# Kernel optimization log

Hardware: AMD Instinct MI355X
Metric: run time of the kernel (lower is better)

The kernel has to match this reference:

```python
import jax, jax.numpy as jnp
import numpy as np

N_S = 4096      # number of sentences
N_K = 8192      # number of knowledge entries
HID = 1024      # settings.hidden_dim
SENT = 1024     # settings.sent_dim


def setup_inputs() -> dict:
    key = jax.random.key(0)
    ks = jax.random.split(key, 6)
    sentences = jax.random.normal(ks[0], (N_S, SENT), dtype=jnp.float32)
    knowledge = jax.random.normal(ks[1], (N_K, 3 * HID), dtype=jnp.float32)
    # Linear params stored as [in, out] for x @ W + b
    Ws = jax.random.normal(ks[2], (SENT, HID), dtype=jnp.float32) * 0.02
    bs = jnp.zeros((HID,), dtype=jnp.float32)
    Wk = jax.random.normal(ks[3], (3 * HID, HID), dtype=jnp.float32) * 0.02
    bk = jnp.zeros((HID,), dtype=jnp.float32)
    return {"sentences": sentences, "knowledge": knowledge,
            "Ws": Ws, "bs": bs, "Wk": Wk, "bk": bk}


def reference(sentences, knowledge, Ws, bs, Wk, bk):
    S = sentences @ Ws + bs                  # [N_s, h]
    K = knowledge @ Wk + bk                  # [N_k, h]
    align_scores = S @ K.T                   # [N_s, N_k]
    # NOTE: softmax over dim=0 (sentence axis), exactly as the torch module
    attentions = jax.nn.softmax(align_scores, axis=0)
    fused = attentions @ knowledge           # [N_s, 3h]
    return (fused, attentions)
```

## Files before the change

kernel.cpp:

```cpp
#include <hip/hip_runtime.h>
#include <hip/hip_bf16.h>
#include <cstdint>
#include <cstddef>

#define N_S 4096
#define N_Kn 8192
#define HID 1024
#define SENT 1024
#define K3 3072

typedef __attribute__((ext_vector_type(4))) float f4;
typedef __attribute__((ext_vector_type(8))) short bf8;
typedef __attribute__((ext_vector_type(4))) short bf4;
typedef unsigned short u16;

__device__ __forceinline__ u16 f2bf(float x) {
    __hip_bfloat16 h = __float2bfloat16(x);
    return __builtin_bit_cast(u16, h);
}
__device__ __forceinline__ float bf2f(u16 u) {
    union { unsigned int u; float f; } v; v.u = ((unsigned int)u) << 16;
    return v.f;
}

__device__ __forceinline__ void gl16(const u16* g, u16* l) {
    __builtin_amdgcn_global_load_lds(
        (const __attribute__((address_space(1))) void*)g,
        (__attribute__((address_space(3))) void*)l, 16, 0, 0);
}

__device__ __forceinline__ int xcd_swz(int bid, int nwg) {
    const int cpx = nwg >> 3;
    return (bid & 7) * cpx + (bid >> 3);
}

__global__ __launch_bounds__(256) void transpose_split_f32(
    const float* __restrict__ in, u16* __restrict__ hi, u16* __restrict__ lo,
    int R, int C)
{
    __shared__ float tile[32][33];
    const int bx = blockIdx.x * 32, by = blockIdx.y * 32;
    const int tx = threadIdx.x & 31, ty = threadIdx.x >> 5;
#pragma unroll
    for (int i = 0; i < 32; i += 8)
        tile[ty + i][tx] = in[(size_t)(by + ty + i) * C + bx + tx];
    __syncthreads();
#pragma unroll
    for (int i = 0; i < 32; i += 8) {
        const float v = tile[tx][ty + i];
        const u16 h = f2bf(v);
        const size_t o = (size_t)(bx + ty + i) * R + by + tx;
        hi[o] = h;
        lo[o] = f2bf(v - bf2f(h));
    }
}

__global__ __launch_bounds__(256) void transpose_f32_bf16(
    const float* __restrict__ in, u16* __restrict__ out, int R, int C)
{
    __shared__ float tile[32][33];
    const int bx = blockIdx.x * 32, by = blockIdx.y * 32;
    const int tx = threadIdx.x & 31, ty = threadIdx.x >> 5;
#pragma unroll
    for (int i = 0; i < 32; i += 8)
        tile[ty + i][tx] = in[(size_t)(by + ty + i) * C + bx + tx];
    __syncthreads();
#pragma unroll
    for (int i = 0; i < 32; i += 8)
        out[(size_t)(bx + ty + i) * R + by + tx] = f2bf(tile[tx][ty + i]);
}

__global__ __launch_bounds__(512, 2) void gemm8(
    const u16* __restrict__ A, const u16* __restrict__ B,
    float* __restrict__ C, int N, int Kd, int gx)
{
    __shared__ u16 sA[2][2][8192];
    __shared__ u16 sB[2][2][8192];

    const int swz = xcd_swz(blockIdx.x, gridDim.x);
    const int bx = swz % gx, by = swz / gx;
    const long brow = (long)by * 256, bcol = (long)bx * 256;

    const int t = threadIdx.x;
    const int w = t >> 6, l = t & 63;
    const int fr = l & 15, kg = l >> 4;
    const int wm = w >> 2;
    const int wn = w & 3;
    const int hb = wn >> 1;
    const int cb = (wn & 1) * 64;

    const int srow = t >> 3;
    const int schk = ((t & 7) ^ (srow & 7)) << 3;
    const int sldb = w << 9;

    auto stage = [&](const u16* g, u16* lds) {
        gl16(g + (long)srow * Kd + schk, lds + sldb);
        gl16(g + (long)(srow + 64) * Kd + schk, lds + 4096 + sldb);
    };

    f4 acc[8][4];
#pragma unroll
    for (int m = 0; m < 8; ++m)
#pragma unroll
        for (int n = 0; n < 4; ++n) acc[m][n] = (f4){0.f, 0.f, 0.f, 0.f};

    auto phase = [&](int buf, int mh, int nh, int stg, long kts, bool wait) {
        bf8 fa[4][2], fb[2][2];
#pragma unroll
        for (int m = 0; m < 4; ++m)
#pragma unroll
            for (int kk = 0; kk < 2; ++kk)
                fa[m][kk] = *(bf8*)&sA[buf][wm][
                    (mh * 64 + m * 16 + fr) * 64 + (((kk << 2) + kg) ^ (fr & 7)) * 8];
#pragma unroll
        for (int nn = 0; nn < 2; ++nn)
#pragma unroll
            for (int kk = 0; kk < 2; ++kk)
                fb[nn][kk] = *(bf8*)&sB[buf][hb][
                    (cb + nh * 32 + nn * 16 + fr) * 64 + (((kk << 2) + kg) ^ (fr & 7)) * 8];
        if (stg == 1) {
            stage(A + brow * Kd + kts, &sA[buf ^ 1][0][0]);
            stage(A + (brow + 128) * Kd + kts, &sA[buf ^ 1][1][0]);
        } else if (stg == 2) {
            stage(B + bcol * Kd + kts, &sB[buf ^ 1][0][0]);
            stage(B + (bcol + 128) * Kd + kts, &sB[buf ^ 1][1][0]);
        }
        __builtin_amdgcn_s_barrier();
        __builtin_amdgcn_s_setprio(1);
#pragma unroll
        for (int kk = 0; kk < 2; ++kk)
#pragma unroll
            for (int m = 0; m < 4; ++m)
#pragma unroll
                for (int nn = 0; nn < 2; ++nn)
                    acc[mh * 4 + m][nh * 2 + nn] = __builtin_amdgcn_mfma_f32_16x16x32_bf16(
                        fa[m][kk], fb[nn][kk], acc[mh * 4 + m][nh * 2 + nn], 0, 0, 0);
        __builtin_amdgcn_s_setprio(0);
        if (wait) asm volatile("s_waitcnt vmcnt(0)" ::: "memory");
        __builtin_amdgcn_s_barrier();
    };

    stage(A + brow * Kd, &sA[0][0][0]);
    stage(A + (brow + 128) * Kd, &sA[0][1][0]);
    stage(B + bcol * Kd, &sB[0][0][0]);
    stage(B + (bcol + 128) * Kd, &sB[0][1][0]);
    asm volatile("s_waitcnt vmcnt(0)" ::: "memory");
    __builtin_amdgcn_s_barrier();

    const int NIT = Kd >> 7;
    for (int it = 0; it < NIT; ++it) {
        const long k1 = ((long)(2 * it + 1)) << 6;
        const long k2 = ((long)(2 * it + 2)) << 6;
        const bool more = (it + 1 < NIT);
        phase(0, 0, 0, 1, k1, false);
        phase(0, 0, 1, 2, k1, false);
        phase(0, 1, 0, 0, 0, false);
        phase(0, 1, 1, 0, 0, true);
        phase(1, 0, 0, more ? 1 : 0, k2, false);
        phase(1, 0, 1, more ? 2 : 0, k2, false);
        phase(1, 1, 0, 0, 0, false);
        phase(1, 1, 1, 0, 0, true);
    }

#pragma unroll
    for (int n = 0; n < 4; ++n) {
        const long c = bcol + wn * 64 + n * 16 + fr;
#pragma unroll
        for (int m = 0; m < 8; ++m) {
            const long r0 = brow + wm * 128 + m * 16 + kg * 4;
#pragma unroll
            for (int r = 0; r < 4; ++r)
                C[(r0 + r) * (long)N + c] = acc[m][n][r];
        }
    }
}

template <bool SPLIT, bool AF32, bool EPIS>
__global__ __launch_bounds__(256) void gemm_mfma(
    const void* __restrict__ Aany, const u16* __restrict__ Alo_,
    const u16* __restrict__ Bhi_, const u16* __restrict__ Blo_,
    float* __restrict__ Cf, u16* __restrict__ Chi, u16* __restrict__ Clo,
    const float* __restrict__ bias, int N, int Kd, int gx)
{
    constexpr int SA = AF32 ? 48 : 32;
    __shared__ u16 sAh[128 * SA];
    __shared__ u16 sAl[SPLIT ? 128 * SA : 8];
    __shared__ u16 sBh[128 * 32];
    __shared__ u16 sBl[SPLIT ? 128 * 32 : 8];

    const int swz = xcd_swz(blockIdx.x, gridDim.x);
    const int nst_x = gx >> 2;
    const int st = swz >> 4, off = swz & 15;
    const int bxi = (st % nst_x) * 4 + (off & 3);
    const int byi = (st / nst_x) * 4 + (off >> 2);

    const int t = threadIdx.x;
    const int w = t >> 6;
    const int l = t & 63;
    const long brow = (long)byi * 128;
    const long bcol = (long)bxi * 128;

    const int grow = l >> 2;
    const int gcol = ((l & 3) ^ ((l >> 3) & 3)) * 8;

    const int wr = (w >> 1) * 64;
    const int wc = (w & 1) * 64;
    const int fr = l & 15;
    const int kg = l >> 4;
    const int kq = (kg ^ ((fr >> 1) & 3)) * 8;

    f4 acc[4][4];
#pragma unroll
    for (int m = 0; m < 4; m++)
#pragma unroll
        for (int n = 0; n < 4; n++) acc[m][n] = (f4){0.f, 0.f, 0.f, 0.f};

    const int nkt = Kd >> 5;
    for (int kt = 0; kt < nkt; ++kt) {
        const int k0 = kt * 32;

#pragma unroll
        for (int i = 0; i < 2; ++i) {
            const long r = bcol + i * 64 + w * 16 + grow;
            const int lb = i * 2048 + w * 512;
            gl16(Bhi_ + r * Kd + k0 + gcol, sBh + lb);
            if constexpr (SPLIT) gl16(Blo_ + r * Kd + k0 + gcol, sBl + lb);
        }

        if constexpr (!AF32) {
            const u16* Ahi = (const u16*)Aany;
#pragma unroll
            for (int i = 0; i < 2; ++i) {
                const long r = brow + i * 64 + w * 16 + grow;
                const int lb = i * 2048 + w * 512;
                gl16(Ahi + r * Kd + k0 + gcol, sAh + lb);
                if constexpr (SPLIT) gl16(Alo_ + r * Kd + k0 + gcol, sAl + lb);
            }
        } else {
            const float* Af = (const float*)Aany;
            const int ar = w * 8 + (l >> 3);
            const int cF = (l & 7) * 4;
#pragma unroll
            for (int j = 0; j < 4; ++j) {
                const int r = j * 32 + ar;
                const f4 v = *(const f4*)(Af + (brow + r) * (long)Kd + k0 + cF);
                u16 h[4], lw[4];
#pragma unroll
                for (int q = 0; q < 4; ++q) {
                    h[q] = f2bf(v[q]);
                    if constexpr (SPLIT) lw[q] = f2bf(v[q] - bf2f(h[q]));
                }
                *(bf4*)&sAh[r * SA + cF] = *(bf4*)h;
                if constexpr (SPLIT) *(bf4*)&sAl[r * SA + cF] = *(bf4*)lw;
            }
        }
        __syncthreads();

        bf8 fah[4], fbh[4], fal[4], fbl[4];
#pragma unroll
        for (int m = 0; m < 4; ++m) {
            if constexpr (AF32) {
                fah[m] = *(bf8*)&sAh[(wr + m * 16 + fr) * SA + kg * 8];
                if constexpr (SPLIT) fal[m] = *(bf8*)&sAl[(wr + m * 16 + fr) * SA + kg * 8];
            } else {
                fah[m] = *(bf8*)&sAh[(wr + m * 16 + fr) * 32 + kq];
                if constexpr (SPLIT) fal[m] = *(bf8*)&sAl[(wr + m * 16 + fr) * 32 + kq];
            }
            fbh[m] = *(bf8*)&sBh[(wc + m * 16 + fr) * 32 + kq];
            if constexpr (SPLIT) fbl[m] = *(bf8*)&sBl[(wc + m * 16 + fr) * 32 + kq];
        }
#pragma unroll
        for (int m = 0; m < 4; ++m)
#pragma unroll
            for (int n = 0; n < 4; ++n) {
                acc[m][n] = __builtin_amdgcn_mfma_f32_16x16x32_bf16(fah[m], fbh[n], acc[m][n], 0, 0, 0);
                if constexpr (SPLIT) {
                    acc[m][n] = __builtin_amdgcn_mfma_f32_16x16x32_bf16(fah[m], fbl[n], acc[m][n], 0, 0, 0);
                    acc[m][n] = __builtin_amdgcn_mfma_f32_16x16x32_bf16(fal[m], fbh[n], acc[m][n], 0, 0, 0);
                }
            }
        __syncthreads();
    }

#pragma unroll
    for (int n = 0; n < 4; ++n) {
        const long c = bcol + wc + n * 16 + fr;
        float bv = 0.f;
        if constexpr (EPIS) bv = bias[c];
#pragma unroll
        for (int m = 0; m < 4; ++m) {
            const long r0 = brow + wr + m * 16 + kg * 4;
#pragma unroll
            for (int r = 0; r < 4; ++r) {
                const float v = acc[m][n][r] + bv;
                if constexpr (EPIS) {
                    const u16 h = f2bf(v);
                    Chi[(r0 + r) * (long)N + c] = h;
                    Clo[(r0 + r) * (long)N + c] = f2bf(v - bf2f(h));
                } else {
                    Cf[(r0 + r) * (long)N + c] = v;
                }
            }
        }
    }
}

#define RCHUNK 128

__global__ __launch_bounds__(256) void softmax_partial(
    const float* __restrict__ align, float* __restrict__ pm, float* __restrict__ ps)
{
    const int col = blockIdx.x * 256 + threadIdx.x;
    const int r0 = blockIdx.y * RCHUNK;
    float m = -3.4e38f;
    for (int r = 0; r < RCHUNK; r++)
        m = fmaxf(m, align[(size_t)(r0 + r) * N_Kn + col]);
    float s = 0.f;
    for (int r = 0; r < RCHUNK; r++)
        s += __expf(align[(size_t)(r0 + r) * N_Kn + col] - m);
    pm[(size_t)blockIdx.y * N_Kn + col] = m;
    ps[(size_t)blockIdx.y * N_Kn + col] = s;
}

__global__ __launch_bounds__(256) void softmax_combine(
    const float* __restrict__ pm, const float* __restrict__ ps,
    float* __restrict__ fm, float* __restrict__ fsinv)
{
    const int col = blockIdx.x * 256 + threadIdx.x;
    float m = -3.4e38f;
#pragma unroll
    for (int i = 0; i < 32; i++) m = fmaxf(m, pm[(size_t)i * N_Kn + col]);
    float s = 0.f;
#pragma unroll
    for (int i = 0; i < 32; i++)
        s += ps[(size_t)i * N_Kn + col] * __expf(pm[(size_t)i * N_Kn + col] - m);
    fm[col] = m;
    fsinv[col] = 1.f / s;
}

__global__ __launch_bounds__(256) void softmax_norm(
    float* __restrict__ align, u16* __restrict__ abf,
    const float* __restrict__ fm, const float* __restrict__ fsinv)
{
    const int col = blockIdx.x * 256 + threadIdx.x;
    const int r0 = blockIdx.y * RCHUNK;
    const float m = fm[col], si = fsinv[col];
    for (int r = 0; r < RCHUNK; r++) {
        const size_t idx = (size_t)(r0 + r) * N_Kn + col;
        const float v = __expf(align[idx] - m) * si;
        align[idx] = v;
        abf[idx] = f2bf(v);
    }
}

extern "C" void kernel_launch(void* const* d_in, const int* in_sizes, int n_in,
                              void* d_out, int out_size, void* d_ws, size_t ws_size,
                              hipStream_t stream)
{
    const float* sentences = (const float*)d_in[0];
    const float* knowledge = (const float*)d_in[1];
    const float* Ws = (const float*)d_in[2];
    const float* bs = (const float*)d_in[3];
    const float* Wk = (const float*)d_in[4];
    const float* bk = (const float*)d_in[5];

    float* out_fused = (float*)d_out;
    float* out_attn = (float*)d_out + (size_t)N_S * K3;

    char* w = (char*)d_ws;
    u16* attn_bf = (u16*)w;
    u16* WsT_hi = (u16*)w; w += (size_t)HID * SENT * 2;
    u16* WsT_lo = (u16*)w; w += (size_t)HID * SENT * 2;
    u16* WkT_hi = (u16*)w; w += (size_t)HID * K3 * 2;
    u16* WkT_lo = (u16*)w; w += (size_t)HID * K3 * 2;
    u16* S_hi   = (u16*)w; w += (size_t)N_S * HID * 2;
    u16* S_lo   = (u16*)w; w += (size_t)N_S * HID * 2;
    u16* K_hi   = (u16*)w; w += (size_t)N_Kn * HID * 2;
    u16* K_lo   = (u16*)w; w += (size_t)N_Kn * HID * 2;
    u16* kT     = (u16*)w; w += (size_t)K3 * N_Kn * 2;
    float* pm   = (float*)w; w += (size_t)32 * N_Kn * 4;
    float* ps   = (float*)w; w += (size_t)32 * N_Kn * 4;
    float* fm   = (float*)w; w += (size_t)N_Kn * 4;
    float* fsv  = (float*)w; w += (size_t)N_Kn * 4;

    transpose_split_f32<<<dim3(HID / 32, SENT / 32), 256, 0, stream>>>(Ws, WsT_hi, WsT_lo, SENT, HID);
    transpose_split_f32<<<dim3(HID / 32, K3 / 32), 256, 0, stream>>>(Wk, WkT_hi, WkT_lo, K3, HID);
    transpose_f32_bf16<<<dim3(K3 / 32, N_Kn / 32), 256, 0, stream>>>(knowledge, kT, N_Kn, K3);

    gemm_mfma<true, true, true><<<(HID / 128) * (N_S / 128), 256, 0, stream>>>(
        sentences, nullptr, WsT_hi, WsT_lo, nullptr, S_hi, S_lo, bs, HID, SENT, HID / 128);

    gemm_mfma<true, true, true><<<(HID / 128) * (N_Kn / 128), 256, 0, stream>>>(
        knowledge, nullptr, WkT_hi, WkT_lo, nullptr, K_hi, K_lo, bk, HID, K3, HID / 128);

    gemm_mfma<true, false, false><<<(N_Kn / 128) * (N_S / 128), 256, 0, stream>>>(
        S_hi, S_lo, K_hi, K_lo, out_attn, nullptr, nullptr, nullptr, N_Kn, HID, N_Kn / 128);

    softmax_partial<<<dim3(N_Kn / 256, N_S / RCHUNK), 256, 0, stream>>>(out_attn, pm, ps);
    softmax_combine<<<dim3(N_Kn / 256), 256, 0, stream>>>(pm, ps, fm, fsv);
    softmax_norm<<<dim3(N_Kn / 256, N_S / RCHUNK), 256, 0, stream>>>(out_attn, attn_bf, fm, fsv);

    gemm8<<<(K3 / 256) * (N_S / 256), 512, 0, stream>>>(
        attn_bf, kT, out_fused, K3, N_Kn, K3 / 256);
}
```

Before: 829.9 us.

## Restructure gemm8 pipeline to prefetch two k-tiles ahead with fragment reuse

Rewrites the gemm8 main loop so global loads for tile k+2 are issued while tile k is computed. Counted vmcnt(8) waits replace full drains, which keeps one tile's loads in flight. B fragments are kept in two register sets and reused across both M halves, so fewer LDS reads are needed per k-tile. The cost is more live registers, and the deeper schedule may raise register pressure under the 512x2 launch bound.

```diff
diff --git a/kernel.cpp b/kernel.cpp
--- a/kernel.cpp
+++ b/kernel.cpp
@@ -69,6 +69,29 @@
     for (int i = 0; i < 32; i += 8)
         out[(size_t)(bx + ty + i) * R + by + tx] = f2bf(tile[tx][ty + i]);
 }
+
+#define G8_LDA(buf, mh) \
+  _Pragma("unroll") for (int m_ = 0; m_ < 4; ++m_) \
+  _Pragma("unroll") for (int kk_ = 0; kk_ < 2; ++kk_) \
+    fa[m_][kk_] = *(const bf8*)&sA[buf][wm][((mh)*64 + m_*16 + fr)*64 + (((kk_*4+kg) ^ (fr&7))<<3)];
+
+#define G8_LDB(buf, nh, FB) \
+  _Pragma("unroll") for (int nn_ = 0; nn_ < 2; ++nn_) \
+  _Pragma("unroll") for (int kk_ = 0; kk_ < 2; ++kk_) \
+    FB[nn_][kk_] = *(const bf8*)&sB[buf][hb][(cb + (nh)*32 + nn_*16 + fr)*64 + (((kk_*4+kg) ^ (fr&7))<<3)];
+
+#define G8_MMA(mh, nh, FB) \
+  _Pragma("unroll") for (int kk_ = 0; kk_ < 2; ++kk_) \
+  _Pragma("unroll") for (int m_ = 0; m_ < 4; ++m_) \
+  _Pragma("unroll") for (int nn_ = 0; nn_ < 2; ++nn_) \
+    acc[(mh)*4+m_][(nh)*2+nn_] = __builtin_amdgcn_mfma_f32_16x16x32_bf16( \
+        fa[m_][kk_], FB[nn_][kk_], acc[(mh)*4+m_][(nh)*2+nn_], 0, 0, 0);
+
+#define BARR __builtin_amdgcn_s_barrier()
+#define PRIO1 __builtin_amdgcn_s_setprio(1)
+#define PRIO0 __builtin_amdgcn_s_setprio(0)
+#define VM8  asm volatile("s_waitcnt vmcnt(8)" ::: "memory")
+#define VM0  asm volatile("s_waitcnt vmcnt(0)" ::: "memory")
 
 __global__ __launch_bounds__(512, 2) void gemm8(
     const u16* __restrict__ A, const u16* __restrict__ B,
@@ -93,10 +116,16 @@
     const int schk = ((t & 7) ^ (srow & 7)) << 3;
     const int sldb = w << 9;
 
-    auto stage = [&](const u16* g, u16* lds) {
-        gl16(g + (long)srow * Kd + schk, lds + sldb);
-        gl16(g + (long)(srow + 64) * Kd + schk, lds + 4096 + sldb);
+    auto stA = [&](int buf, int h, int kt) {
+        const u16* g = A + (brow + h * 128 + srow) * (long)Kd + ((long)kt << 6) + schk;
+        gl16(g, &sA[buf][h][sldb]);
+        gl16(g + 64 * (long)Kd, &sA[buf][h][4096 + sldb]);
     };
+    auto stB = [&](int buf, int h, int kt) {
+        const u16* g = B + (bcol + h * 128 + srow) * (long)Kd + ((long)kt << 6) + schk;
+        gl16(g, &sB[buf][h][sldb]);
+        gl16(g + 64 * (long)Kd, &sB[buf][h][4096 + sldb]);
+    };
 
     f4 acc[8][4];
 #pragma unroll
@@ -104,62 +133,42 @@
 #pragma unroll
         for (int n = 0; n < 4; ++n) acc[m][n] = (f4){0.f, 0.f, 0.f, 0.f};
 
-    auto phase = [&](int buf, int mh, int nh, int stg, long kts, bool wait) {
-        bf8 fa[4][2], fb[2][2];
-#pragma unroll
-        for (int m = 0; m < 4; ++m)
-#pragma unroll
-            for (int kk = 0; kk < 2; ++kk)
-                fa[m][kk] = *(bf8*)&sA[buf][wm][
-                    (mh * 64 + m * 16 + fr) * 64 + (((kk << 2) + kg) ^ (fr & 7)) * 8];
-#pragma unroll
-        for (int nn = 0; nn < 2; ++nn)
-#pragma unroll
-            for (int kk = 0; kk < 2; ++kk)
-                fb[nn][kk] = *(bf8*)&sB[buf][hb][
-                    (cb + nh * 32 + nn * 16 + fr) * 64 + (((kk << 2) + kg) ^ (fr & 7)) * 8];
-        if (stg == 1) {
-            stage(A + brow * Kd + kts, &sA[buf ^ 1][0][0]);
-            stage(A + (brow + 128) * Kd + kts, &sA[buf ^ 1][1][0]);
-        } else if (stg == 2) {
-            stage(B + bcol * Kd + kts, &sB[buf ^ 1][0][0]);
-            stage(B + (bcol + 128) * Kd + kts, &sB[buf ^ 1][1][0]);
-        }
-        __builtin_amdgcn_s_barrier();
-        __builtin_amdgcn_s_setprio(1);
-#pragma unroll
-        for (int kk = 0; kk < 2; ++kk)
-#pragma unroll
-            for (int m = 0; m < 4; ++m)
-#pragma unroll
-                for (int nn = 0; nn < 2; ++nn)
-                    acc[mh * 4 + m][nh * 2 + nn] = __builtin_amdgcn_mfma_f32_16x16x32_bf16(
-                        fa[m][kk], fb[nn][kk], acc[mh * 4 + m][nh * 2 + nn], 0, 0, 0);
-        __builtin_amdgcn_s_setprio(0);
-        if (wait) asm volatile("s_waitcnt vmcnt(0)" ::: "memory");
-        __builtin_amdgcn_s_barrier();
-    };
-
-    stage(A + brow * Kd, &sA[0][0][0]);
-    stage(A + (brow + 128) * Kd, &sA[0][1][0]);
-    stage(B + bcol * Kd, &sB[0][0][0]);
-    stage(B + (bcol + 128) * Kd, &sB[0][1][0]);
-    asm volatile("s_waitcnt vmcnt(0)" ::: "memory");
-    __builtin_amdgcn_s_barrier();
-
-    const int NIT = Kd >> 7;
-    for (int it = 0; it < NIT; ++it) {
-        const long k1 = ((long)(2 * it + 1)) << 6;
-        const long k2 = ((long)(2 * it + 2)) << 6;
-        const bool more = (it + 1 < NIT);
-        phase(0, 0, 0, 1, k1, false);
-        phase(0, 0, 1, 2, k1, false);
-        phase(0, 1, 0, 0, 0, false);
-        phase(0, 1, 1, 0, 0, true);
-        phase(1, 0, 0, more ? 1 : 0, k2, false);
-        phase(1, 0, 1, more ? 2 : 0, k2, false);
-        phase(1, 1, 0, 0, 0, false);
-        phase(1, 1, 1, 0, 0, true);
+    bf8 fa[4][2], fb0[2][2], fb1[2][2];
+
+    const int NK = Kd >> 6;
+
+    stB(0, 0, 0); stB(0, 1, 0); stA(0, 0, 0); stA(0, 1, 0);
+    stB(1, 0, 1); stB(1, 1, 1); stA(1, 0, 1); stA(1, 1, 1);
+    VM8;
+    BARR;
+
+    for (int it = 0; it < (NK >> 1); ++it) {
+        const int t2 = 2 * it + 2, t3 = 2 * it + 3;
+        const bool s2 = t2 < NK, s3 = t3 < NK;
+
+        G8_LDA(0, 0); G8_LDB(0, 0, fb0);
+        BARR; PRIO1; G8_MMA(0, 0, fb0); PRIO0; BARR;
+        G8_LDB(0, 1, fb1);
+        BARR; PRIO1; G8_MMA(0, 1, fb1); PRIO0; BARR;
+        G8_LDA(0, 1);
+        if (s2) { stB(0, 0, t2); stB(0, 1, t2); }
+        BARR; PRIO1; G8_MMA(1, 0, fb0); PRIO0; BARR;
+        if (s2) { stA(0, 0, t2); stA(0, 1, t2); }
+        BARR; PRIO1; G8_MMA(1, 1, fb1); PRIO0;
+        if (s2) { VM8; } else { VM0; }
+        BARR;
+
+        G8_LDA(1, 0); G8_LDB(1, 0, fb0);
+        BARR; PRIO1; G8_MMA(0, 0, fb0); PRIO0; BARR;
+        G8_LDB(1, 1, fb1);
+        BARR; PRIO1; G8_MMA(0, 1, fb1); PRIO0; BARR;
+        G8_LDA(1, 1);
+        if (s3) { stB(1, 0, t3); stB(1, 1, t3); }
+        BARR; PRIO1; G8_MMA(1, 0, fb0); PRIO0; BARR;
+        if (s3) { stA(1, 0, t3); stA(1, 1, t3); }
+        BARR; PRIO1; G8_MMA(1, 1, fb1); PRIO0;
+        if (s3) { VM8; } else { VM0; }
+        BARR;
     }
 
 #pragma unroll
```

Result: faster. 783.5 us (-5.6%).
